# Kernel tuning notes

Measured on AMD Instinct MI355X. Metric: run time of the kernel, lower is better.

Reference implementation:

```python
import jax, jax.numpy as jnp
import numpy as np

EPS = 1e-5


def hyper_graph_conv(x, elements, W, b):
    """x: [B, C, N] vertex features; elements: [M, 8] vertex ids per hex element.
    Gather 8 vertex features per element, apply Linear(8C -> 8Co) on the
    concatenated features, then scatter-mean the 8 outputs back to vertices.
    Returns [B, Co, N]."""
    B, C, N = x.shape
    M = elements.shape[0]
    Co = W.shape[0] // 8
    g = x[:, :, elements]                      # [B, C, M, 8]
    g = jnp.transpose(g, (0, 2, 3, 1)).reshape(B, M, 8 * C)   # [B, M, 8C]
    h = jnp.einsum('bmk,ok->bmo', g, W) + b    # [B, M, 8Co]
    h = h.reshape(B, M * 8, Co)                # per-(element,corner) vertex outputs
    flat = elements.reshape(-1)                # [M*8]
    out = jnp.zeros((B, N, Co), dtype=x.dtype).at[:, flat, :].add(h)
    cnt = jnp.zeros((N,), dtype=x.dtype).at[flat].add(1.0)
    out = out / jnp.maximum(cnt, 1.0)[None, :, None]
    return jnp.transpose(out, (0, 2, 1))       # [B, Co, N]


def batch_norm(x, gamma, beta):
    # BatchNorm1d in training mode over [B, C, N]: stats over (B, N)
    mean = jnp.mean(x, axis=(0, 2), keepdims=True)
    var = jnp.mean(jnp.square(x - mean), axis=(0, 2), keepdims=True)
    xn = (x - mean) * jax.lax.rsqrt(var + EPS)
    return xn * gamma[None, :, None] + beta[None, :, None]


def setup_inputs() -> dict:
    key = jax.random.key(0)
    ks = jax.random.split(key, 8)
    B, Cin, Cout, N, M = 4, 8, 16, 100000, 98304
    return {
        'x': jax.random.normal(ks[0], (B, Cin, N), dtype=jnp.float32),
        'elements': jax.random.randint(ks[1], (M, 8), 0, N, dtype=jnp.int32),
        'W1': jax.random.normal(ks[2], (8 * Cout, 8 * Cin), dtype=jnp.float32) * (1.0 / np.sqrt(8 * Cin)),
        'b1': jnp.zeros((8 * Cout,), dtype=jnp.float32),
        'gamma1': jnp.ones((Cout,), dtype=jnp.float32),
        'beta1': jnp.zeros((Cout,), dtype=jnp.float32),
        'W2': jax.random.normal(ks[3], (8 * Cout, 8 * Cout), dtype=jnp.float32) * (1.0 / np.sqrt(8 * Cout)),
        'b2': jnp.zeros((8 * Cout,), dtype=jnp.float32),
        'gamma2': jnp.ones((Cout,), dtype=jnp.float32),
        'beta2': jnp.zeros((Cout,), dtype=jnp.float32),
        'Wskip': jax.random.normal(ks[4], (Cout, Cin), dtype=jnp.float32) * (1.0 / np.sqrt(Cin)),
        'bskip': jnp.zeros((Cout,), dtype=jnp.float32),
    }


def reference(x, elements, W1, b1, gamma1, beta1, W2, b2, gamma2, beta2, Wskip, bskip):
    out = hyper_graph_conv(x, elements, W1, b1)        # [B, Cout, N]
    out = jax.nn.relu(batch_norm(out, gamma1, beta1))
    out = hyper_graph_conv(out, elements, W2, b2)      # [B, Cout, N]
    out = batch_norm(out, gamma2, beta2)
    skip = jnp.einsum('bcn,oc->bon', x, Wskip) + bskip[None, :, None]  # Conv1d k=1
    out = jax.nn.relu(out + skip)
    return out
```

## Files before the change

### kernel.cpp

```cpp
#include <hip/hip_runtime.h>

#define NB 4
#define CIN 8
#define CO 16
#define NV 100000
#define NVP 100096
#define NM 98304
#define NPOS (NM*8)
#define NBLK ((NV+255)/256)
#define VPW 14
#define REDB 1786

typedef short s16x8 __attribute__((ext_vector_type(8)));
typedef float f32x4 __attribute__((ext_vector_type(4)));
typedef unsigned short u16;
typedef unsigned int u32;

#define OFF_STAT  800256
#define OFF_ROWS  800640
#define OFF_BSUM  1200768
#define OFF_POS   1202432
#define OFF_XTB   4348160
#define OFF_W1B   10748160
#define OFF_W2B   10764544
#define OFF_H1    10797312
#define OFF_MBUF  23597312
#define OFF_HBUF  49197312
#define OFF_CNTR  149860608
#define OFF_BASER (OFF_CNTR + 8*NVP*4)
#define WS_NEED   (OFF_BASER + 8*NVP*4)

static __device__ __forceinline__ u16 f2bf(float f){
  union { float f; u32 u; } v; v.f = f;
  u32 r = v.u + 0x7fffu + ((v.u >> 16) & 1u);
  return (u16)(r >> 16);
}
static __device__ __forceinline__ float bf2f_lo(u32 w){
  union { u32 u; float f; } v; v.u = w << 16; return v.f;
}
static __device__ __forceinline__ float bf2f_hi(u32 w){
  union { u32 u; float f; } v; v.u = w & 0xffff0000u; return v.f;
}
static __device__ __forceinline__ u32 pk2(float a, float b){
  return (u32)f2bf(a) | (((u32)f2bf(b)) << 16);
}

__global__ __launch_bounds__(256) void k_xt(const float* __restrict__ x, u16* __restrict__ xtb)
{
  __shared__ float tile[32][257];
  int t = threadIdx.x;
  int v0 = blockIdx.x*256;
  #pragma unroll
  for (int r = 0; r < 32; r++){
    int v = v0 + t;
    tile[r][t] = (v < NV) ? x[(size_t)r*NV + v] : 0.f;
  }
  __syncthreads();
  int v = v0 + t;
  if (v < NV){
    u16 o[32] __attribute__((aligned(16)));
    #pragma unroll
    for (int r = 0; r < 32; r++) o[r] = f2bf(tile[r][t]);
    uint4* dst = (uint4*)(xtb + (size_t)v*32);
    #pragma unroll
    for (int k = 0; k < 4; k++) dst[k] = *(uint4*)(o + k*8);
  }
}

__global__ __launch_bounds__(256) void k_slot(const int* __restrict__ elem,
    const float* __restrict__ W1, const float* __restrict__ W2,
    int* __restrict__ cntR, int* __restrict__ slot,
    u16* __restrict__ w1b, u16* __restrict__ w2b)
{
  int b = blockIdx.x;
  if (b >= 1024){
    const int T1 = 128*64, T2 = T1 + 128*128;
    for (int i = (b - 1024)*256 + threadIdx.x; i < T2; i += 8*256){
      if (i < T1) w1b[i] = f2bf(W1[i]);
      else { int j = i - T1; w2b[j] = f2bf(W2[j]); }
    }
    return;
  }
  int* myc = cntR + (b & 7)*NVP;
  int i0 = b*768 + threadIdx.x;
  #pragma unroll
  for (int k = 0; k < 3; k++){
    int i = i0 + k*256;
    int v = elem[i];
    slot[i] = atomicAdd(myc + v, 1);
  }
}

__global__ __launch_bounds__(256) void k_scan_a(const int* __restrict__ cntR, int* __restrict__ bsum)
{
  int v = blockIdx.x*256 + threadIdx.x;
  int x = 0;
  if (v < NV){
    #pragma unroll
    for (int r = 0; r < 8; r++) x += cntR[r*NVP + v];
  }
  #pragma unroll
  for (int off = 32; off > 0; off >>= 1) x += __shfl_down(x, off);
  __shared__ int ls[4];
  int wid = threadIdx.x >> 6, lane = threadIdx.x & 63;
  if (lane == 0) ls[wid] = x;
  __syncthreads();
  if (threadIdx.x == 0) bsum[blockIdx.x] = ls[0] + ls[1] + ls[2] + ls[3];
}

__global__ __launch_bounds__(256) void k_scan_c(const int* __restrict__ cntR,
    const int* __restrict__ bsum, int* __restrict__ rows, int* __restrict__ baseR)
{
  int wid = threadIdx.x >> 6, lane = threadIdx.x & 63;
  int v = blockIdx.x*256 + threadIdx.x;
  int cr[8];
  #pragma unroll
  for (int r = 0; r < 8; r++) cr[r] = (v < NV) ? cntR[r*NVP + v] : 0;
  int pre[8]; int x = 0;
  #pragma unroll
  for (int r = 0; r < 8; r++){ pre[r] = x; x += cr[r]; }
  int incl = x;
  #pragma unroll
  for (int off = 1; off <= 32; off <<= 1){
    int y = __shfl_up(incl, off);
    if (lane >= off) incl += y;
  }
  __shared__ int wt[4];
  __shared__ int sbase;
  if (lane == 63) wt[wid] = incl;
  if (threadIdx.x < 64){
    int s = 0;
    for (int i = threadIdx.x; i < blockIdx.x; i += 64) s += bsum[i];
    #pragma unroll
    for (int off = 32; off > 0; off >>= 1) s += __shfl_down(s, off);
    if (threadIdx.x == 0) sbase = s;
  }
  __syncthreads();
  int woff = 0;
  for (int w = 0; w < 4; w++) if (w < wid) woff += wt[w];
  if (v < NV){
    int row0 = sbase + woff + incl - x;
    rows[v] = row0;
    #pragma unroll
    for (int r = 0; r < 8; r++) baseR[r*NVP + v] = row0 + pre[r];
  }
}

__global__ __launch_bounds__(256) void k_pos2(const int* __restrict__ elem,
    const int* __restrict__ baseR, int* __restrict__ pos)
{
  int i4 = blockIdx.x*256 + threadIdx.x;
  int4 e = ((const int4*)elem)[i4];
  int4 s = ((const int4*)pos)[i4];
  int r = ((i4*4)/768) & 7;
  const int* br = baseR + r*NVP;
  int4 p;
  p.x = br[e.x] + s.x;
  p.y = br[e.y] + s.y;
  p.z = br[e.z] + s.z;
  p.w = br[e.w] + s.w;
  ((int4*)pos)[i4] = p;
}

__global__ __launch_bounds__(256) void k_conv1(const int* __restrict__ elem,
    const u16* __restrict__ xtb, const u16* __restrict__ w1b,
    const float* __restrict__ b1, const int* __restrict__ pos, u16* __restrict__ hbuf)
{
  const int lane = threadIdx.x & 63;
  const int col = lane & 15, kg = lane >> 4, b = lane & 3;
  s16x8 wf[8][2];
  #pragma unroll
  for (int j2 = 0; j2 < 8; j2++)
    #pragma unroll
    for (int t = 0; t < 2; t++)
      wf[j2][t] = *(const s16x8*)(w1b + (j2*16 + col)*64 + t*32 + kg*8);
  float bb[8];
  #pragma unroll
  for (int j2 = 0; j2 < 8; j2++) bb[j2] = b1[j2*16 + col];

  int wave = (int)((blockIdx.x*blockDim.x + threadIdx.x) >> 6);
  int g0 = wave, g1 = wave + 12288;
  int ma0 = g0*4 + (col >> 2), ma1 = g1*4 + (col >> 2);
  int me0 = g0*4 + kg,         me1 = g1*4 + kg;

  int e00 = elem[ma0*8 + kg], e01 = elem[ma0*8 + 4 + kg];
  int e10 = elem[ma1*8 + kg], e11 = elem[ma1*8 + 4 + kg];
  int4 p0l = *(const int4*)(pos + me0*8), p0h = *(const int4*)(pos + me0*8 + 4);
  int4 p1l = *(const int4*)(pos + me1*8), p1h = *(const int4*)(pos + me1*8 + 4);
  s16x8 a00 = *(const s16x8*)(xtb + (size_t)e00*32 + b*8);
  s16x8 a01 = *(const s16x8*)(xtb + (size_t)e01*32 + b*8);
  s16x8 a10 = *(const s16x8*)(xtb + (size_t)e10*32 + b*8);
  s16x8 a11 = *(const s16x8*)(xtb + (size_t)e11*32 + b*8);

  int pe0[8] = {p0l.x,p0l.y,p0l.z,p0l.w,p0h.x,p0h.y,p0h.z,p0h.w};
  int pe1[8] = {p1l.x,p1l.y,p1l.z,p1l.w,p1h.x,p1h.y,p1h.z,p1h.w};

  #pragma unroll
  for (int j2 = 0; j2 < 8; j2++){
    f32x4 c = {0.f,0.f,0.f,0.f};
    c = __builtin_amdgcn_mfma_f32_16x16x32_bf16(a00, wf[j2][0], c, 0, 0, 0);
    c = __builtin_amdgcn_mfma_f32_16x16x32_bf16(a01, wf[j2][1], c, 0, 0, 0);
    uint2 d; d.x = pk2(c[0]+bb[j2], c[1]+bb[j2]); d.y = pk2(c[2]+bb[j2], c[3]+bb[j2]);
    *(uint2*)(hbuf + (size_t)pe0[j2]*64 + col*4) = d;
  }
  #pragma unroll
  for (int j2 = 0; j2 < 8; j2++){
    f32x4 c = {0.f,0.f,0.f,0.f};
    c = __builtin_amdgcn_mfma_f32_16x16x32_bf16(a10, wf[j2][0], c, 0, 0, 0);
    c = __builtin_amdgcn_mfma_f32_16x16x32_bf16(a11, wf[j2][1], c, 0, 0, 0);
    uint2 d; d.x = pk2(c[0]+bb[j2], c[1]+bb[j2]); d.y = pk2(c[2]+bb[j2], c[3]+bb[j2]);
    *(uint2*)(hbuf + (size_t)pe1[j2]*64 + col*4) = d;
  }
}

__global__ __launch_bounds__(256) void k_conv2(const int* __restrict__ elem,
    const u16* __restrict__ h1, const u16* __restrict__ w2b,
    const float* __restrict__ b2, const int* __restrict__ pos, u16* __restrict__ hbuf)
{
  __shared__ u16 wl[16384];
  #pragma unroll
  for (int r = 0; r < 8; r++){
    int q = threadIdx.x + 256*r;
    int j2t = q >> 6, ln = q & 63;
    int cc = ln & 15, kk = ln >> 4;
    int j2 = j2t >> 2, tt = j2t & 3;
    *(s16x8*)(wl + (size_t)q*8) =
        *(const s16x8*)(w2b + (j2*16 + cc)*128 + tt*32 + kk*8);
  }

  const int lane = threadIdx.x & 63;
  const int col = lane & 15, kg = lane >> 4, b = lane & 3;
  const int p = kg >> 1;
  const int c0 = (kg & 1)*8;
  float bb[8];
  #pragma unroll
  for (int j2 = 0; j2 < 8; j2++) bb[j2] = b2[j2*16 + col];

  int wave = (int)((blockIdx.x*blockDim.x + threadIdx.x) >> 6);
  int g0 = wave, g1 = wave + 12288;
  int ma0 = g0*4 + (col >> 2), ma1 = g1*4 + (col >> 2);
  int me0 = g0*4 + kg,         me1 = g1*4 + kg;

  int4 e0l = *(const int4*)(elem + ma0*8), e0h = *(const int4*)(elem + ma0*8 + 4);
  int4 e1l = *(const int4*)(elem + ma1*8), e1h = *(const int4*)(elem + ma1*8 + 4);
  int4 p0l = *(const int4*)(pos + me0*8),  p0h = *(const int4*)(pos + me0*8 + 4);
  int4 p1l = *(const int4*)(pos + me1*8),  p1h = *(const int4*)(pos + me1*8 + 4);

  int v00 = p ? e0l.y : e0l.x, v01 = p ? e0l.w : e0l.z;
  int v02 = p ? e0h.y : e0h.x, v03 = p ? e0h.w : e0h.z;
  int v10 = p ? e1l.y : e1l.x, v11 = p ? e1l.w : e1l.z;
  int v12 = p ? e1h.y : e1h.x, v13 = p ? e1h.w : e1h.z;

  s16x8 af0[4], af1[4];
  af0[0] = *(const s16x8*)(h1 + (size_t)v00*64 + b*16 + c0);
  af0[1] = *(const s16x8*)(h1 + (size_t)v01*64 + b*16 + c0);
  af0[2] = *(const s16x8*)(h1 + (size_t)v02*64 + b*16 + c0);
  af0[3] = *(const s16x8*)(h1 + (size_t)v03*64 + b*16 + c0);
  af1[0] = *(const s16x8*)(h1 + (size_t)v10*64 + b*16 + c0);
  af1[1] = *(const s16x8*)(h1 + (size_t)v11*64 + b*16 + c0);
  af1[2] = *(const s16x8*)(h1 + (size_t)v12*64 + b*16 + c0);
  af1[3] = *(const s16x8*)(h1 + (size_t)v13*64 + b*16 + c0);

  int pe0[8] = {p0l.x,p0l.y,p0l.z,p0l.w,p0h.x,p0h.y,p0h.z,p0h.w};
  int pe1[8] = {p1l.x,p1l.y,p1l.z,p1l.w,p1h.x,p1h.y,p1h.z,p1h.w};

  __syncthreads();

  #pragma unroll
  for (int j2 = 0; j2 < 8; j2++){
    s16x8 w0 = *(const s16x8*)(wl + ((size_t)(j2*4 + 0)*64 + lane)*8);
    s16x8 w1 = *(const s16x8*)(wl + ((size_t)(j2*4 + 1)*64 + lane)*8);
    s16x8 w2 = *(const s16x8*)(wl + ((size_t)(j2*4 + 2)*64 + lane)*8);
    s16x8 w3 = *(const s16x8*)(wl + ((size_t)(j2*4 + 3)*64 + lane)*8);
    f32x4 c = {0.f,0.f,0.f,0.f};
    c = __builtin_amdgcn_mfma_f32_16x16x32_bf16(af0[0], w0, c, 0, 0, 0);
    c = __builtin_amdgcn_mfma_f32_16x16x32_bf16(af0[1], w1, c, 0, 0, 0);
    c = __builtin_amdgcn_mfma_f32_16x16x32_bf16(af0[2], w2, c, 0, 0, 0);
    c = __builtin_amdgcn_mfma_f32_16x16x32_bf16(af0[3], w3, c, 0, 0, 0);
    uint2 d; d.x = pk2(c[0]+bb[j2], c[1]+bb[j2]); d.y = pk2(c[2]+bb[j2], c[3]+bb[j2]);
    *(uint2*)(hbuf + (size_t)pe0[j2]*64 + col*4) = d;
  }
  #pragma unroll
  for (int j2 = 0; j2 < 8; j2++){
    s16x8 w0 = *(const s16x8*)(wl + ((size_t)(j2*4 + 0)*64 + lane)*8);
    s16x8 w1 = *(const s16x8*)(wl + ((size_t)(j2*4 + 1)*64 + lane)*8);
    s16x8 w2 = *(const s16x8*)(wl + ((size_t)(j2*4 + 2)*64 + lane)*8);
    s16x8 w3 = *(const s16x8*)(wl + ((size_t)(j2*4 + 3)*64 + lane)*8);
    f32x4 c = {0.f,0.f,0.f,0.f};
    c = __builtin_amdgcn_mfma_f32_16x16x32_bf16(af1[0], w0, c, 0, 0, 0);
    c = __builtin_amdgcn_mfma_f32_16x16x32_bf16(af1[1], w1, c, 0, 0, 0);
    c = __builtin_amdgcn_mfma_f32_16x16x32_bf16(af1[2], w2, c, 0, 0, 0);
    c = __builtin_amdgcn_mfma_f32_16x16x32_bf16(af1[3], w3, c, 0, 0, 0);
    uint2 d; d.x = pk2(c[0]+bb[j2], c[1]+bb[j2]); d.y = pk2(c[2]+bb[j2], c[3]+bb[j2]);
    *(uint2*)(hbuf + (size_t)pe1[j2]*64 + col*4) = d;
  }
}

__global__ __launch_bounds__(256) void k_reduce(const u16* __restrict__ hbuf,
    const int* __restrict__ rows, u16* __restrict__ mbuf, float* __restrict__ stat)
{
  int lane = threadIdx.x & 63, wid = threadIdx.x >> 6;
  int half = lane >> 5;
  int hl   = lane & 31;
  int k8   = lane & 7;
  int rg   = (lane >> 3) & 3;
  int w = (blockIdx.x*blockDim.x + threadIdx.x) >> 6;
  int v0 = w * VPW;

  int vv = v0 + lane;
  int rr = 0;
  if (lane < VPW + 1) rr = (vv < NV) ? rows[vv] : NPOS;

  int rs[7], ce[7];
  #pragma unroll
  for (int j = 0; j < 7; j++){
    rs[j] = __shfl(rr, 2*j + half);
    ce[j] = __shfl(rr, 2*j + half + 1) - rs[j];
  }

  uint4 d0[7], d1[7];
  #pragma unroll
  for (int j = 0; j < 7; j++){
    uint4 z = {0u,0u,0u,0u};
    d0[j] = z; d1[j] = z;
    const u16* base = hbuf + (size_t)rs[j]*64 + hl*8;
    if (rg     < ce[j]) d0[j] = *(const uint4*)(base);
    if (4 + rg < ce[j]) d1[j] = *(const uint4*)(base + 4*64);
  }

  float st_s0 = 0.f, st_q0 = 0.f, st_s1 = 0.f, st_q1 = 0.f;

  #pragma unroll
  for (int j = 0; j < 7; j++){
    float a0,a1,a2,a3,a4,a5,a6,a7;
    {
      uint4 dA = d0[j], dB = d1[j];
      a0 = bf2f_lo(dA.x)+bf2f_lo(dB.x); a1 = bf2f_hi(dA.x)+bf2f_hi(dB.x);
      a2 = bf2f_lo(dA.y)+bf2f_lo(dB.y); a3 = bf2f_hi(dA.y)+bf2f_hi(dB.y);
      a4 = bf2f_lo(dA.z)+bf2f_lo(dB.z); a5 = bf2f_hi(dA.z)+bf2f_hi(dB.z);
      a6 = bf2f_lo(dA.w)+bf2f_lo(dB.w); a7 = bf2f_hi(dA.w)+bf2f_hi(dB.w);
    }
    for (int p = 8; p < ce[j]; p += 4){
      uint4 d = {0u,0u,0u,0u};
      if (p + rg < ce[j]) d = *(const uint4*)(hbuf + (size_t)(rs[j]+p)*64 + hl*8);
      a0 += bf2f_lo(d.x); a1 += bf2f_hi(d.x); a2 += bf2f_lo(d.y); a3 += bf2f_hi(d.y);
      a4 += bf2f_lo(d.z); a5 += bf2f_hi(d.z); a6 += bf2f_lo(d.w); a7 += bf2f_hi(d.w);
    }
    #pragma unroll
    for (int off = 8; off <= 16; off <<= 1){
      a0 += __shfl_xor(a0, off); a1 += __shfl_xor(a1, off);
      a2 += __shfl_xor(a2, off); a3 += __shfl_xor(a3, off);
      a4 += __shfl_xor(a4, off); a5 += __shfl_xor(a5, off);
      a6 += __shfl_xor(a6, off); a7 += __shfl_xor(a7, off);
    }
    int v = v0 + 2*j + half;
    if (hl < 8 && v < NV){
      float inv = 1.0f / fmaxf((float)ce[j], 1.0f);
      float c0b[4] = {a0*inv, a1*inv, a2*inv, a3*inv};
      float c1b[4] = {a4*inv, a5*inv, a6*inv, a7*inv};
      #pragma unroll
      for (int q = 0; q < 4; q++){
        *(u32*)(mbuf + (size_t)v*64 + q*16 + 2*k8) = pk2(c0b[q], c1b[q]);
        st_s0 += c0b[q]; st_q0 += c0b[q]*c0b[q];
        st_s1 += c1b[q]; st_q1 += c1b[q]*c1b[q];
      }
    }
  }

  st_s0 += __shfl_xor(st_s0, 32); st_q0 += __shfl_xor(st_q0, 32);
  st_s1 += __shfl_xor(st_s1, 32); st_q1 += __shfl_xor(st_q1, 32);
  __shared__ float ls[4][16], lq[4][16];
  if (lane < 8){
    ls[wid][2*k8] = st_s0; ls[wid][2*k8+1] = st_s1;
    lq[wid][2*k8] = st_q0; lq[wid][2*k8+1] = st_q1;
  }
  __syncthreads();
  if (threadIdx.x < 32){
    int c2 = threadIdx.x & 15, which = threadIdx.x >> 4;
    float tot = 0.f;
    #pragma unroll
    for (int w2 = 0; w2 < 4; w2++) tot += which ? lq[w2][c2] : ls[w2][c2];
    unsafeAtomicAdd(stat + which*16 + c2, tot);
  }
}

__global__ __launch_bounds__(256) void k_apply1(const u16* __restrict__ mbuf,
    const float* __restrict__ stat, const float* __restrict__ gamma,
    const float* __restrict__ beta, u16* __restrict__ h1)
{
  __shared__ float sc[16], sh[16];
  if (threadIdx.x < 16){
    int co = threadIdx.x;
    const float invn = 1.0f / (float)(NB*NV);
    float m = stat[co]*invn;
    float var = stat[16+co]*invn - m*m;
    float s = gamma[co]*rsqrtf(var + 1e-5f);
    sc[co] = s; sh[co] = beta[co] - m*s;
  }
  __syncthreads();
  int idx = blockIdx.x*256 + threadIdx.x;
  int v = idx >> 2, b = idx & 3;
  if (v >= NV) return;
  const uint4* src = (const uint4*)(mbuf + (size_t)v*64 + b*16);
  uint4 m0 = src[0], m1 = src[1];
  u32 mw[8] = {m0.x,m0.y,m0.z,m0.w,m1.x,m1.y,m1.z,m1.w};
  u16 o[16] __attribute__((aligned(16)));
  #pragma unroll
  for (int k = 0; k < 8; k++){
    int c0 = 2*k, c1 = 2*k + 1;
    float va = bf2f_lo(mw[k])*sc[c0] + sh[c0];
    float vb = bf2f_hi(mw[k])*sc[c1] + sh[c1];
    o[c0] = f2bf(fmaxf(va, 0.f));
    o[c1] = f2bf(fmaxf(vb, 0.f));
  }
  uint4* dst = (uint4*)(h1 + (size_t)v*64 + b*16);
  dst[0] = *(uint4*)(o);
  dst[1] = *(uint4*)(o + 8);
}

__global__ __launch_bounds__(256) void k_final(const u16* __restrict__ mbuf,
    const float* __restrict__ stat, const float* __restrict__ gamma,
    const float* __restrict__ beta, const float* __restrict__ x,
    const float* __restrict__ wsk, const float* __restrict__ bsk, float* __restrict__ out)
{
  __shared__ float sc[16], sh[16];
  if (threadIdx.x < 16){
    int co = threadIdx.x;
    const float invn = 1.0f / (float)(NB*NV);
    float m = stat[co]*invn;
    float var = stat[16+co]*invn - m*m;
    float s = gamma[co]*rsqrtf(var + 1e-5f);
    sc[co] = s; sh[co] = beta[co] - m*s + bsk[co];
  }
  __syncthreads();
  int n = blockIdx.x*blockDim.x + threadIdx.x;
  int b = blockIdx.y;
  if (n >= NV) return;
  float xv[8];
  #pragma unroll
  for (int c = 0; c < 8; c++) xv[c] = x[((size_t)b*8 + c)*NV + n];
  const uint4* src = (const uint4*)(mbuf + (size_t)n*64 + b*16);
  uint4 m0 = src[0], m1 = src[1];
  u32 mw[8] = {m0.x,m0.y,m0.z,m0.w,m1.x,m1.y,m1.z,m1.w};
  #pragma unroll
  for (int k = 0; k < 8; k++){
    #pragma unroll
    for (int h = 0; h < 2; h++){
      int co = 2*k + h;
      float val = (h ? bf2f_hi(mw[k]) : bf2f_lo(mw[k]))*sc[co] + sh[co];
      #pragma unroll
      for (int c = 0; c < 8; c++) val += wsk[co*8+c]*xv[c];
      out[((size_t)b*16 + co)*NV + n] = fmaxf(val, 0.f);
    }
  }
}

extern "C" void kernel_launch(void* const* d_in, const int* in_sizes, int n_in,
                              void* d_out, int out_size, void* d_ws, size_t ws_size,
                              hipStream_t stream) {
  const float* x    = (const float*)d_in[0];
  const int*   elem = (const int*)  d_in[1];
  const float* W1   = (const float*)d_in[2];
  const float* b1   = (const float*)d_in[3];
  const float* g1   = (const float*)d_in[4];
  const float* be1  = (const float*)d_in[5];
  const float* W2   = (const float*)d_in[6];
  const float* b2   = (const float*)d_in[7];
  const float* g2   = (const float*)d_in[8];
  const float* be2  = (const float*)d_in[9];
  const float* Wsk  = (const float*)d_in[10];
  const float* bsk  = (const float*)d_in[11];
  float* out = (float*)d_out;

  if (ws_size < (size_t)WS_NEED) return;

  char* ws = (char*)d_ws;
  float* stat  = (float*)(ws + OFF_STAT);
  int*   rows  = (int*)  (ws + OFF_ROWS);
  int*   bsum  = (int*)  (ws + OFF_BSUM);
  int*   pos   = (int*)  (ws + OFF_POS);
  u16*   xtb   = (u16*)  (ws + OFF_XTB);
  u16*   w1b   = (u16*)  (ws + OFF_W1B);
  u16*   w2b   = (u16*)  (ws + OFF_W2B);
  u16*   h1    = (u16*)  (ws + OFF_H1);
  u16*   mbuf  = (u16*)  (ws + OFF_MBUF);
  u16*   hbuf  = (u16*)  (ws + OFF_HBUF);
  int*   cntR  = (int*)  (ws + OFF_CNTR);
  int*   baseR = (int*)  (ws + OFF_BASER);

  hipMemsetAsync(ws + OFF_CNTR, 0, 8*NVP*4, stream);
  hipMemsetAsync(ws + OFF_STAT, 0, 384, stream);

  k_xt<<<NBLK, 256, 0, stream>>>(x, xtb);
  k_slot<<<1032, 256, 0, stream>>>(elem, W1, W2, cntR, pos, w1b, w2b);
  k_scan_a<<<NBLK, 256, 0, stream>>>(cntR, bsum);
  k_scan_c<<<NBLK, 256, 0, stream>>>(cntR, bsum, rows, baseR);
  k_pos2<<<768, 256, 0, stream>>>(elem, baseR, pos);

  k_conv1<<<3072, 256, 0, stream>>>(elem, xtb, w1b, b1, pos, hbuf);
  k_reduce<<<REDB, 256, 0, stream>>>(hbuf, rows, mbuf, stat);
  k_apply1<<<(NV*4 + 255)/256, 256, 0, stream>>>(mbuf, stat, g1, be1, h1);

  k_conv2<<<3072, 256, 0, stream>>>(elem, h1, w2b, b2, pos, hbuf);
  k_reduce<<<REDB, 256, 0, stream>>>(hbuf, rows, mbuf, stat + 32);
  k_final<<<dim3((NV+255)/256, NB), 256, 0, stream>>>(mbuf, stat + 32, g2, be2, x, Wsk, bsk, out);
}
```

Before: 239.1 us.

## Fuse BN1+ReLU into conv2 gather, drop apply kernel and stat memset

Removes the separate k_apply1 pass by applying the first batch-norm scale/shift and ReLU to gathered raw features inside k_conv2, eliminating a full read/write of the h1 buffer. Moves weight conversion and stat zeroing into extra blocks of k_xt, dropping a memset launch. Also widens the reduce prologue to preload three row-groups before the loop. Cost: conv2 repeats the BN/ReLU math on each gathered value (about eight times per vertex) and adds an extra rounding through bf16.

Measured after the change: 224.2 us. -6.2%, faster.

```diff
diff --git a/kernel.cpp b/kernel.cpp
--- a/kernel.cpp
+++ b/kernel.cpp
@@ -23,7 +23,6 @@
 #define OFF_XTB   4348160
 #define OFF_W1B   10748160
 #define OFF_W2B   10764544
-#define OFF_H1    10797312
 #define OFF_MBUF  23597312
 #define OFF_HBUF  49197312
 #define OFF_CNTR  149860608
@@ -41,13 +40,28 @@
 static __device__ __forceinline__ float bf2f_hi(u32 w){
   union { u32 u; float f; } v; v.u = w & 0xffff0000u; return v.f;
 }
+static __device__ __forceinline__ float bf2f16(u16 h){
+  union { u32 u; float f; } v; v.u = ((u32)h) << 16; return v.f;
+}
 static __device__ __forceinline__ u32 pk2(float a, float b){
   return (u32)f2bf(a) | (((u32)f2bf(b)) << 16);
 }
 
-__global__ __launch_bounds__(256) void k_xt(const float* __restrict__ x, u16* __restrict__ xtb)
+__global__ __launch_bounds__(256) void k_xt(const float* __restrict__ x, u16* __restrict__ xtb,
+    const float* __restrict__ W1, const float* __restrict__ W2,
+    u16* __restrict__ w1b, u16* __restrict__ w2b, float* __restrict__ stat)
 {
   __shared__ float tile[32][257];
+  if (blockIdx.x >= NBLK){
+    int b3 = blockIdx.x - NBLK;
+    if (b3 == 0 && threadIdx.x < 64) stat[threadIdx.x] = 0.f;
+    const int T1 = 128*64, T2 = T1 + 128*128;
+    for (int i = b3*256 + threadIdx.x; i < T2; i += 8*256){
+      if (i < T1) w1b[i] = f2bf(W1[i]);
+      else { int j = i - T1; w2b[j] = f2bf(W2[j]); }
+    }
+    return;
+  }
   int t = threadIdx.x;
   int v0 = blockIdx.x*256;
   #pragma unroll
@@ -68,19 +82,9 @@
 }
 
 __global__ __launch_bounds__(256) void k_slot(const int* __restrict__ elem,
-    const float* __restrict__ W1, const float* __restrict__ W2,
-    int* __restrict__ cntR, int* __restrict__ slot,
-    u16* __restrict__ w1b, u16* __restrict__ w2b)
+    int* __restrict__ cntR, int* __restrict__ slot)
 {
   int b = blockIdx.x;
-  if (b >= 1024){
-    const int T1 = 128*64, T2 = T1 + 128*128;
-    for (int i = (b - 1024)*256 + threadIdx.x; i < T2; i += 8*256){
-      if (i < T1) w1b[i] = f2bf(W1[i]);
-      else { int j = i - T1; w2b[j] = f2bf(W2[j]); }
-    }
-    return;
-  }
   int* myc = cntR + (b & 7)*NVP;
   int i0 = b*768 + threadIdx.x;
   #pragma unroll
@@ -214,10 +218,13 @@
 }
 
 __global__ __launch_bounds__(256) void k_conv2(const int* __restrict__ elem,
-    const u16* __restrict__ h1, const u16* __restrict__ w2b,
-    const float* __restrict__ b2, const int* __restrict__ pos, u16* __restrict__ hbuf)
+    const u16* __restrict__ mbuf, const u16* __restrict__ w2b,
+    const float* __restrict__ b2, const float* __restrict__ stat,
+    const float* __restrict__ gamma, const float* __restrict__ beta,
+    const int* __restrict__ pos, u16* __restrict__ hbuf)
 {
   __shared__ u16 wl[16384];
+  __shared__ float sc[16], sh[16];
   #pragma unroll
   for (int r = 0; r < 8; r++){
     int q = threadIdx.x + 256*r;
@@ -227,6 +234,14 @@
     *(s16x8*)(wl + (size_t)q*8) =
         *(const s16x8*)(w2b + (j2*16 + cc)*128 + tt*32 + kk*8);
   }
+  if (threadIdx.x < 16){
+    int co = threadIdx.x;
+    const float invn = 1.0f / (float)(NB*NV);
+    float m = stat[co]*invn;
+    float var = stat[16+co]*invn - m*m;
+    float s = gamma[co]*rsqrtf(var + 1e-5f);
+    sc[co] = s; sh[co] = beta[co] - m*s;
+  }
 
   const int lane = threadIdx.x & 63;
   const int col = lane & 15, kg = lane >> 4, b = lane & 3;
@@ -252,19 +267,36 @@
   int v12 = p ? e1h.y : e1h.x, v13 = p ? e1h.w : e1h.z;
 
   s16x8 af0[4], af1[4];
-  af0[0] = *(const s16x8*)(h1 + (size_t)v00*64 + b*16 + c0);
-  af0[1] = *(const s16x8*)(h1 + (size_t)v01*64 + b*16 + c0);
-  af0[2] = *(const s16x8*)(h1 + (size_t)v02*64 + b*16 + c0);
-  af0[3] = *(const s16x8*)(h1 + (size_t)v03*64 + b*16 + c0);
-  af1[0] = *(const s16x8*)(h1 + (size_t)v10*64 + b*16 + c0);
-  af1[1] = *(const s16x8*)(h1 + (size_t)v11*64 + b*16 + c0);
-  af1[2] = *(const s16x8*)(h1 + (size_t)v12*64 + b*16 + c0);
-  af1[3] = *(const s16x8*)(h1 + (size_t)v13*64 + b*16 + c0);
+  af0[0] = *(const s16x8*)(mbuf + (size_t)v00*64 + b*16 + c0);
+  af0[1] = *(const s16x8*)(mbuf + (size_t)v01*64 + b*16 + c0);
+  af0[2] = *(const s16x8*)(mbuf + (size_t)v02*64 + b*16 + c0);
+  af0[3] = *(const s16x8*)(mbuf + (size_t)v03*64 + b*16 + c0);
+  af1[0] = *(const s16x8*)(mbuf + (size_t)v10*64 + b*16 + c0);
+  af1[1] = *(const s16x8*)(mbuf + (size_t)v11*64 + b*16 + c0);
+  af1[2] = *(const s16x8*)(mbuf + (size_t)v12*64 + b*16 + c0);
+  af1[3] = *(const s16x8*)(mbuf + (size_t)v13*64 + b*16 + c0);
 
   int pe0[8] = {p0l.x,p0l.y,p0l.z,p0l.w,p0h.x,p0h.y,p0h.z,p0h.w};
   int pe1[8] = {p1l.x,p1l.y,p1l.z,p1l.w,p1h.x,p1h.y,p1h.z,p1h.w};
 
   __syncthreads();
+
+  #pragma unroll
+  for (int t = 0; t < 4; t++){
+    u32 r0[4], r1[4];
+    #pragma unroll
+    for (int ii = 0; ii < 4; ii++){
+      int ca = c0 + 2*ii, cb = ca + 1;
+      float x0 = bf2f16((u16)af0[t][2*ii])   * sc[ca] + sh[ca];
+      float x1 = bf2f16((u16)af0[t][2*ii+1]) * sc[cb] + sh[cb];
+      float y0 = bf2f16((u16)af1[t][2*ii])   * sc[ca] + sh[ca];
+      float y1 = bf2f16((u16)af1[t][2*ii+1]) * sc[cb] + sh[cb];
+      r0[ii] = pk2(fmaxf(x0, 0.f), fmaxf(x1, 0.f));
+      r1[ii] = pk2(fmaxf(y0, 0.f), fmaxf(y1, 0.f));
+    }
+    af0[t] = *(s16x8*)r0;
+    af1[t] = *(s16x8*)r1;
+  }
 
   #pragma unroll
   for (int j2 = 0; j2 < 8; j2++){
@@ -318,14 +350,15 @@
     ce[j] = __shfl(rr, 2*j + half + 1) - rs[j];
   }
 
-  uint4 d0[7], d1[7];
+  uint4 d0[7], d1[7], d2[7];
   #pragma unroll
   for (int j = 0; j < 7; j++){
     uint4 z = {0u,0u,0u,0u};
-    d0[j] = z; d1[j] = z;
+    d0[j] = z; d1[j] = z; d2[j] = z;
     const u16* base = hbuf + (size_t)rs[j]*64 + hl*8;
     if (rg     < ce[j]) d0[j] = *(const uint4*)(base);
     if (4 + rg < ce[j]) d1[j] = *(const uint4*)(base + 4*64);
+    if (8 + rg < ce[j]) d2[j] = *(const uint4*)(base + 8*64);
   }
 
   float st_s0 = 0.f, st_q0 = 0.f, st_s1 = 0.f, st_q1 = 0.f;
@@ -334,13 +367,17 @@
   for (int j = 0; j < 7; j++){
     float a0,a1,a2,a3,a4,a5,a6,a7;
     {
-      uint4 dA = d0[j], dB = d1[j];
-      a0 = bf2f_lo(dA.x)+bf2f_lo(dB.x); a1 = bf2f_hi(dA.x)+bf2f_hi(dB.x);
-      a2 = bf2f_lo(dA.y)+bf2f_lo(dB.y); a3 = bf2f_hi(dA.y)+bf2f_hi(dB.y);
-      a4 = bf2f_lo(dA.z)+bf2f_lo(dB.z); a5 = bf2f_hi(dA.z)+bf2f_hi(dB.z);
-      a6 = bf2f_lo(dA.w)+bf2f_lo(dB.w); a7 = bf2f_hi(dA.w)+bf2f_hi(dB.w);
-    }
-    for (int p = 8; p < ce[j]; p += 4){
+      uint4 dA = d0[j], dB = d1[j], dC = d2[j];
+      a0 = bf2f_lo(dA.x)+bf2f_lo(dB.x)+bf2f_lo(dC.x);
+      a1 = bf2f_hi(dA.x)+bf2f_hi(dB.x)+bf2f_hi(dC.x);
+      a2 = bf2f_lo(dA.y)+bf2f_lo(dB.y)+bf2f_lo(dC.y);
+      a3 = bf2f_hi(dA.y)+bf2f_hi(dB.y)+bf2f_hi(dC.y);
+      a4 = bf2f_lo(dA.z)+bf2f_lo(dB.z)+bf2f_lo(dC.z);
+      a5 = bf2f_hi(dA.z)+bf2f_hi(dB.z)+bf2f_hi(dC.z);
+      a6 = bf2f_lo(dA.w)+bf2f_lo(dB.w)+bf2f_lo(dC.w);
+      a7 = bf2f_hi(dA.w)+bf2f_hi(dB.w)+bf2f_hi(dC.w);
+    }
+    for (int p = 12; p < ce[j]; p += 4){
       uint4 d = {0u,0u,0u,0u};
       if (p + rg < ce[j]) d = *(const uint4*)(hbuf + (size_t)(rs[j]+p)*64 + hl*8);
       a0 += bf2f_lo(d.x); a1 += bf2f_hi(d.x); a2 += bf2f_lo(d.y); a3 += bf2f_hi(d.y);
@@ -382,40 +419,6 @@
     for (int w2 = 0; w2 < 4; w2++) tot += which ? lq[w2][c2] : ls[w2][c2];
     unsafeAtomicAdd(stat + which*16 + c2, tot);
   }
-}
-
-__global__ __launch_bounds__(256) void k_apply1(const u16* __restrict__ mbuf,
-    const float* __restrict__ stat, const float* __restrict__ gamma,
-    const float* __restrict__ beta, u16* __restrict__ h1)
-{
-  __shared__ float sc[16], sh[16];
-  if (threadIdx.x < 16){
-    int co = threadIdx.x;
-    const float invn = 1.0f / (float)(NB*NV);
-    float m = stat[co]*invn;
-    float var = stat[16+co]*invn - m*m;
-    float s = gamma[co]*rsqrtf(var + 1e-5f);
-    sc[co] = s; sh[co] = beta[co] - m*s;
-  }
-  __syncthreads();
-  int idx = blockIdx.x*256 + threadIdx.x;
-  int v = idx >> 2, b = idx & 3;
-  if (v >= NV) return;
-  const uint4* src = (const uint4*)(mbuf + (size_t)v*64 + b*16);
-  uint4 m0 = src[0], m1 = src[1];
-  u32 mw[8] = {m0.x,m0.y,m0.z,m0.w,m1.x,m1.y,m1.z,m1.w};
-  u16 o[16] __attribute__((aligned(16)));
-  #pragma unroll
-  for (int k = 0; k < 8; k++){
-    int c0 = 2*k, c1 = 2*k + 1;
-    float va = bf2f_lo(mw[k])*sc[c0] + sh[c0];
-    float vb = bf2f_hi(mw[k])*sc[c1] + sh[c1];
-    o[c0] = f2bf(fmaxf(va, 0.f));
-    o[c1] = f2bf(fmaxf(vb, 0.f));
-  }
-  uint4* dst = (uint4*)(h1 + (size_t)v*64 + b*16);
-  dst[0] = *(uint4*)(o);
-  dst[1] = *(uint4*)(o + 8);
 }
 
 __global__ __launch_bounds__(256) void k_final(const u16* __restrict__ mbuf,
@@ -482,26 +485,23 @@
   u16*   xtb   = (u16*)  (ws + OFF_XTB);
   u16*   w1b   = (u16*)  (ws + OFF_W1B);
   u16*   w2b   = (u16*)  (ws + OFF_W2B);
-  u16*   h1    = (u16*)  (ws + OFF_H1);
   u16*   mbuf  = (u16*)  (ws + OFF_MBUF);
   u16*   hbuf  = (u16*)  (ws + OFF_HBUF);
   int*   cntR  = (int*)  (ws + OFF_CNTR);
   int*   baseR = (int*)  (ws + OFF_BASER);
 
   hipMemsetAsync(ws + OFF_CNTR, 0, 8*NVP*4, stream);
-  hipMemsetAsync(ws + OFF_STAT, 0, 384, stream);
-
-  k_xt<<<NBLK, 256, 0, stream>>>(x, xtb);
-  k_slot<<<1032, 256, 0, stream>>>(elem, W1, W2, cntR, pos, w1b, w2b);
+
+  k_xt<<<NBLK + 8, 256, 0, stream>>>(x, xtb, W1, W2, w1b, w2b, stat);
+  k_slot<<<1024, 256, 0, stream>>>(elem, cntR, pos);
   k_scan_a<<<NBLK, 256, 0, stream>>>(cntR, bsum);
   k_scan_c<<<NBLK, 256, 0, stream>>>(cntR, bsum, rows, baseR);
   k_pos2<<<768, 256, 0, stream>>>(elem, baseR, pos);
 
   k_conv1<<<3072, 256, 0, stream>>>(elem, xtb, w1b, b1, pos, hbuf);
   k_reduce<<<REDB, 256, 0, stream>>>(hbuf, rows, mbuf, stat);
-  k_apply1<<<(NV*4 + 255)/256, 256, 0, stream>>>(mbuf, stat, g1, be1, h1);
-
-  k_conv2<<<3072, 256, 0, stream>>>(elem, h1, w2b, b2, pos, hbuf);
+
+  k_conv2<<<3072, 256, 0, stream>>>(elem, mbuf, w2b, b2, stat, g1, be1, pos, hbuf);
   k_reduce<<<REDB, 256, 0, stream>>>(hbuf, rows, mbuf, stat + 32);
   k_final<<<dim3((NV+255)/256, NB), 256, 0, stream>>>(mbuf, stat + 32, g2, be2, x, Wsk, bsk, out);
 }
```
